# Optimization experiments

Hardware: AMD Instinct MI355X
Metric: run time of the kernel (lower is better)

Reference implementation:

```python
import jax, jax.numpy as jnp
import numpy as np

B, NB, S, K, M, C = 2, 6000, 3, 8, 6, 256
INIT = 0.02


def setup_inputs() -> dict:
    key = jax.random.key(0)
    ks = jax.random.split(key, 24)
    d = {}
    d["pts_query_feats"] = jax.random.normal(ks[0], (B, NB, C), jnp.float32)
    d["pts_query_pe"] = jax.random.normal(ks[1], (B, NB, C), jnp.float32)
    d["knn_feat_seq"] = jax.random.normal(ks[2], (S, B, NB, K, C), jnp.float32)
    d["knn_pe_seq"] = jax.random.normal(ks[3], (S, B, NB, K, C), jnp.float32)
    d["sampled_feat"] = jax.random.normal(ks[4], (B, NB, M, C), jnp.float32)
    d["mask"] = jax.random.bernoulli(ks[5], 0.7, (B, NB, M))  # True = valid image sample
    # per-seq temporal attention params (S cloned single-head MHA modules)
    d["Wq_t"] = INIT * jax.random.normal(ks[6], (S, C, C), jnp.float32)
    d["Wk_t"] = INIT * jax.random.normal(ks[7], (S, C, C), jnp.float32)
    d["Wv_t"] = INIT * jax.random.normal(ks[8], (S, C, C), jnp.float32)
    d["Wo_t"] = INIT * jax.random.normal(ks[9], (S, C, C), jnp.float32)
    d["bq_t"] = jnp.zeros((S, C), jnp.float32)
    d["bk_t"] = jnp.zeros((S, C), jnp.float32)
    d["bv_t"] = jnp.zeros((S, C), jnp.float32)
    d["bo_t"] = jnp.zeros((S, C), jnp.float32)
    # cross-sensor single-head MHA params
    d["Wq_c"] = INIT * jax.random.normal(ks[10], (C, C), jnp.float32)
    d["Wk_c"] = INIT * jax.random.normal(ks[11], (C, C), jnp.float32)
    d["Wv_c"] = INIT * jax.random.normal(ks[12], (C, C), jnp.float32)
    d["Wo_c"] = INIT * jax.random.normal(ks[13], (C, C), jnp.float32)
    d["bq_c"] = jnp.zeros((C,), jnp.float32)
    d["bk_c"] = jnp.zeros((C,), jnp.float32)
    d["bv_c"] = jnp.zeros((C,), jnp.float32)
    d["bo_c"] = jnp.zeros((C,), jnp.float32)
    return d


def reference(pts_query_feats, pts_query_pe, knn_feat_seq, knn_pe_seq,
              sampled_feat, mask,
              Wq_t, Wk_t, Wv_t, Wo_t, bq_t, bk_t, bv_t, bo_t,
              Wq_c, Wk_c, Wv_c, Wo_c, bq_c, bk_c, bv_c, bo_c):
    scale = 1.0 / np.sqrt(C).astype(np.float32)

    # with_pos_embed
    q_base = pts_query_feats + pts_query_pe           # [B,NB,C]
    kv = knn_feat_seq + knn_pe_seq                    # [S,B,NB,K,C]

    # temporal attention: per voxel, 1 query token attends over K knn keys;
    # S distinct (cloned) single-head MHA modules, outputs summed over seq.
    q = jnp.einsum('bnc,scd->sbnd', q_base, Wq_t) + bq_t[:, None, None, :]
    k = jnp.einsum('sbnkc,scd->sbnkd', kv, Wk_t) + bk_t[:, None, None, None, :]
    v = jnp.einsum('sbnkc,scd->sbnkd', kv, Wv_t) + bv_t[:, None, None, None, :]
    scores = jnp.einsum('sbnd,sbnkd->sbnk', q, k) * scale
    attn = jax.nn.softmax(scores, axis=-1)
    ctx = jnp.einsum('sbnk,sbnkd->sbnd', attn, v)
    out_s = jnp.einsum('sbnd,sde->sbne', ctx, Wo_t) + bo_t[:, None, None, :]
    out = out_s.sum(axis=0)                           # [B,NB,C]

    # cross-sensor attention over M image samples; attn_mask = ~mask (True blocks)
    valid = mask.any(axis=-1)                         # [B,NB]
    qc = out @ Wq_c + bq_c                            # [B,NB,C]
    kc = sampled_feat @ Wk_c + bk_c                   # [B,NB,M,C]
    vc = sampled_feat @ Wv_c + bv_c
    sc = jnp.einsum('bnc,bnmc->bnm', qc, kc) * scale
    sc = jnp.where(mask, sc, -1e9)
    a = jax.nn.softmax(sc, axis=-1)
    cctx = jnp.einsum('bnm,bnmc->bnc', a, vc)
    outc = cctx @ Wo_c + bo_c                         # [B,NB,C]

    # original drops invalid voxels; we keep static shape and zero them
    return jnp.where(valid[..., None], outc, 0.0)
```

## Files before the change

kernel.cpp:

```cpp
#include <hip/hip_runtime.h>
#include <math.h>

#define CC 256
#define KK 8
#define MM 6
#define SS 3
#define NVOX 12000
#define VB 16
#define NBLK (NVOX / VB)

typedef __attribute__((ext_vector_type(8))) short bf16x8;
typedef __attribute__((ext_vector_type(4))) float f32x4;
typedef __attribute__((ext_vector_type(4))) float fvec4;

#define OFF_QK3PK  0u
#define OFF_WBIGPK 393216u
#define OFF_WVOCPK 786432u
#define OFF_BQK    917504u
#define OFF_BBIG   920576u
#define OFF_BVOC   921600u
#define WS_NEED    922624u

__device__ __forceinline__ float wred(float p) {
  #pragma unroll
  for (int off = 32; off; off >>= 1) p += __shfl_xor(p, off, 64);
  return p;
}
__device__ __forceinline__ uint f2bf(float x) {
  const uint u = __float_as_uint(x);
  return (u + 0x7fffu + ((u >> 16) & 1u)) >> 16;
}
__device__ __forceinline__ uint bfpack(float a, float b) {
  return (f2bf(b) << 16) | f2bf(a);
}
__device__ __forceinline__ float bflo(uint w) { return __uint_as_float(w << 16); }
__device__ __forceinline__ float bfhi(uint w) { return __uint_as_float(w & 0xffff0000u); }

__device__ __forceinline__ f32x4 mfma16(bf16x8 a, bf16x8 b, f32x4 c) {
  return __builtin_amdgcn_mfma_f32_16x16x32_bf16(a, b, c, 0, 0, 0);
}

__global__ __launch_bounds__(256) void prep_all(
    const float* __restrict__ Wq_t, const float* __restrict__ Wq_c,
    const float* __restrict__ Wk_t, const float* __restrict__ Wk_c,
    const float* __restrict__ Wv_t, const float* __restrict__ Wv_c,
    const float* __restrict__ Wo_t, const float* __restrict__ Wo_c,
    const float* __restrict__ bq_t, const float* __restrict__ bq_c,
    const float* __restrict__ bv_t, const float* __restrict__ bv_c,
    const float* __restrict__ bo_t, const float* __restrict__ bo_c,
    uint4* __restrict__ qk3pk, uint4* __restrict__ wbigpk,
    uint4* __restrict__ wvocpk,
    float* __restrict__ bqk, float* __restrict__ bbig,
    float* __restrict__ bvoc) {
  const int b = blockIdx.x, t = threadIdx.x;
  __shared__ float xl[8][256];
  if (b < 96) {
    const int u = b >> 5, c0 = (b & 31) * 8;
    const float* Wq = Wq_t + u * 65536;
    const float* Wk = Wk_t + u * 65536;
    #pragma unroll
    for (int i = 0; i < 8; ++i) xl[i][t] = Wq[(c0 + i) * 256 + t];
    __syncthreads();
    float acc[8] = {0.f, 0.f, 0.f, 0.f, 0.f, 0.f, 0.f, 0.f};
    const float4* wr = (const float4*)(Wk + t * 256);
    #pragma unroll 4
    for (int d4 = 0; d4 < 64; ++d4) {
      const float4 wv = wr[d4];
      #pragma unroll
      for (int j = 0; j < 8; ++j)
        acc[j] += xl[j][d4 * 4] * wv.x + xl[j][d4 * 4 + 1] * wv.y +
                  xl[j][d4 * 4 + 2] * wv.z + xl[j][d4 * 4 + 3] * wv.w;
    }
    const int lane = (((c0 >> 3) & 3) << 4) | (t & 15);
    uint4 o;
    o.x = bfpack(acc[0], acc[1]); o.y = bfpack(acc[2], acc[3]);
    o.z = bfpack(acc[4], acc[5]); o.w = bfpack(acc[6], acc[7]);
    qk3pk[((u * 16 + (t >> 4)) * 8 + (c0 >> 5)) * 64 + lane] = o;
  } else if (b < 192) {
    const int v = (b - 96) >> 5, bi = (b - 96) & 31;
    const int c0 = bi * 8, row0 = v * 256 + c0;
    const float* Wv = Wv_t + v * 65536;
    const float* Wo = Wo_t + v * 65536;
    #pragma unroll
    for (int i = 0; i < 8; ++i) xl[i][t] = Wv[(c0 + i) * 256 + t];
    __syncthreads();
    float a1[8] = {0.f, 0.f, 0.f, 0.f, 0.f, 0.f, 0.f, 0.f};
    #pragma unroll 4
    for (int d = 0; d < 256; ++d) {
      const float w = Wo[d * 256 + t];
      #pragma unroll
      for (int j = 0; j < 8; ++j) a1[j] += xl[j][d] * w;
    }
    __syncthreads();
    #pragma unroll
    for (int j = 0; j < 8; ++j) xl[j][t] = a1[j];
    __syncthreads();
    float a2[8] = {0.f, 0.f, 0.f, 0.f, 0.f, 0.f, 0.f, 0.f};
    #pragma unroll 4
    for (int d = 0; d < 256; ++d) {
      const float w = Wq_c[d * 256 + t];
      #pragma unroll
      for (int j = 0; j < 8; ++j) a2[j] += xl[j][d] * w;
    }
    __syncthreads();
    #pragma unroll
    for (int j = 0; j < 8; ++j) xl[j][t] = a2[j];
    __syncthreads();
    float a3[8] = {0.f, 0.f, 0.f, 0.f, 0.f, 0.f, 0.f, 0.f};
    const float4* wr = (const float4*)(Wk_c + t * 256);
    #pragma unroll 4
    for (int d4 = 0; d4 < 64; ++d4) {
      const float4 wv = wr[d4];
      #pragma unroll
      for (int j = 0; j < 8; ++j)
        a3[j] += xl[j][d4 * 4] * wv.x + xl[j][d4 * 4 + 1] * wv.y +
                 xl[j][d4 * 4 + 2] * wv.z + xl[j][d4 * 4 + 3] * wv.w;
    }
    const int lane = (((row0 >> 3) & 3) << 4) | (t & 15);
    uint4 o;
    o.x = bfpack(a3[0], a3[1]); o.y = bfpack(a3[2], a3[3]);
    o.z = bfpack(a3[4], a3[5]); o.w = bfpack(a3[6], a3[7]);
    wbigpk[((t >> 4) * 24 + (row0 >> 5)) * 64 + lane] = o;
  } else if (b < 224) {
    const int c0 = (b - 192) * 8;
    #pragma unroll
    for (int i = 0; i < 8; ++i) xl[i][t] = Wv_c[(c0 + i) * 256 + t];
    __syncthreads();
    float acc[8] = {0.f, 0.f, 0.f, 0.f, 0.f, 0.f, 0.f, 0.f};
    #pragma unroll 4
    for (int d = 0; d < 256; ++d) {
      const float w = Wo_c[d * 256 + t];
      #pragma unroll
      for (int j = 0; j < 8; ++j) acc[j] += xl[j][d] * w;
    }
    const int lane = (((c0 >> 3) & 3) << 4) | (t & 15);
    uint4 o;
    o.x = bfpack(acc[0], acc[1]); o.y = bfpack(acc[2], acc[3]);
    o.z = bfpack(acc[4], acc[5]); o.w = bfpack(acc[6], acc[7]);
    wvocpk[((t >> 4) * 8 + (c0 >> 5)) * 64 + lane] = o;
  } else if (b < 227) {
    const int u = b - 224;
    xl[0][t] = bq_t[u * 256 + t];
    __syncthreads();
    const float4* wr = (const float4*)(Wk_t + u * 65536 + t * 256);
    float a = 0.f;
    #pragma unroll 4
    for (int d4 = 0; d4 < 64; ++d4) {
      const float4 wv = wr[d4];
      a += xl[0][d4 * 4] * wv.x + xl[0][d4 * 4 + 1] * wv.y +
           xl[0][d4 * 4 + 2] * wv.z + xl[0][d4 * 4 + 3] * wv.w;
    }
    bqk[u * 256 + t] = a;
  } else {
    xl[0][t] = bv_t[t]; xl[1][t] = bv_t[256 + t];
    xl[2][t] = bv_t[512 + t]; xl[3][t] = bv_c[t];
    __syncthreads();
    float bvs = bo_t[t] + bo_t[256 + t] + bo_t[512 + t];
    float bvc = bo_c[t];
    #pragma unroll 2
    for (int d = 0; d < 256; ++d) {
      bvs += xl[0][d] * Wo_t[d * 256 + t] +
             xl[1][d] * Wo_t[65536 + d * 256 + t] +
             xl[2][d] * Wo_t[131072 + d * 256 + t];
      bvc += xl[3][d] * Wo_c[d * 256 + t];
    }
    bvoc[t] = bvc;
    __syncthreads();
    xl[4][t] = bvs;
    __syncthreads();
    float y = bq_c[t];
    #pragma unroll 4
    for (int d = 0; d < 256; ++d) y += xl[4][d] * Wq_c[d * 256 + t];
    __syncthreads();
    xl[5][t] = y;
    __syncthreads();
    const float4* wr = (const float4*)(Wk_c + t * 256);
    float bb = 0.f;
    #pragma unroll 4
    for (int d4 = 0; d4 < 64; ++d4) {
      const float4 wv = wr[d4];
      bb += xl[5][d4 * 4] * wv.x + xl[5][d4 * 4 + 1] * wv.y +
            xl[5][d4 * 4 + 2] * wv.z + xl[5][d4 * 4 + 3] * wv.w;
    }
    bbig[t] = bb;
  }
}

__global__ __launch_bounds__(512, 6) void stftr_mega(
    const float* __restrict__ ptsf, const float* __restrict__ ptspe,
    const float* __restrict__ knnf, const float* __restrict__ knnpe,
    const float* __restrict__ sfeat, const int* __restrict__ maskp,
    const bf16x8* __restrict__ qk3pk, const bf16x8* __restrict__ wbigpk,
    const bf16x8* __restrict__ wvocpk,
    const float* __restrict__ bqk, const float* __restrict__ bbig,
    const float* __restrict__ bvoc,
    float* __restrict__ out) {
  __shared__ char shA[25088];
  __shared__ char shB[24832];
  __shared__ int mlds[VB * MM];
  __shared__ int vlds[VB];
  const int t = threadIdx.x, lane = t & 63, w = t >> 6;
  const int g0 = blockIdx.x * VB;

  {
    uint* qb_u = (uint*)shB;
    const fvec4* a4 = (const fvec4*)(ptsf + (size_t)g0 * CC);
    const fvec4* b4 = (const fvec4*)(ptspe + (size_t)g0 * CC);
    #pragma unroll
    for (int it = 0; it < 2; ++it) {
      const int idx = it * 512 + t;
      const int row = idx >> 6, c4 = idx & 63;
      const fvec4 va = __builtin_nontemporal_load(&a4[idx]);
      const fvec4 vb = __builtin_nontemporal_load(&b4[idx]);
      qb_u[row * 132 + c4 * 2]     = bfpack(va.x + vb.x, va.y + vb.y);
      qb_u[row * 132 + c4 * 2 + 1] = bfpack(va.z + vb.z, va.w + vb.w);
    }
    if (t < VB * MM) mlds[t] = maskp[g0 * MM + t];
  }
  __syncthreads();
  {
    f32x4 acc[6];
    #pragma unroll
    for (int nb = 0; nb < 6; ++nb) acc[nb] = (f32x4){0.f, 0.f, 0.f, 0.f};
    const char* qbase = shB + (lane & 15) * 528 + (lane >> 4) * 16;
    #pragma unroll
    for (int kb = 0; kb < 8; ++kb) {
      const bf16x8 a = *(const bf16x8*)(qbase + kb * 64);
      #pragma unroll
      for (int nb = 0; nb < 6; ++nb) {
        const bf16x8 bb = qk3pk[((w * 6 + nb) * 8 + kb) * 64 + lane];
        acc[nb] = mfma16(a, bb, acc[nb]);
      }
    }
    ushort* us = (ushort*)shA;
    #pragma unroll
    for (int nb = 0; nb < 6; ++nb) {
      const int n = (w * 6 + nb) * 16 + (lane & 15);
      const float bias = bqk[n];
      #pragma unroll
      for (int r = 0; r < 4; ++r) {
        const int row = (lane >> 4) * 4 + r;
        us[row * 776 + n] = (ushort)f2bf(acc[nb][r] + bias);
      }
    }
  }
  __syncthreads();
  {
    const uint* Au = (const uint*)shA;
    uint* Bu = (uint*)shB;
    const fvec4* kfp = (const fvec4*)knnf;
    const fvec4* kpp = (const fvec4*)knnpe;
    for (int q = 0; q < 6; ++q) {
      const int tid = w * 6 + q;
      const int s = tid >> 4, j = tid & 15;
      const size_t rb = ((size_t)(s * NVOX + g0 + j)) * 512 + lane;
      fvec4 sm[KK];
      #pragma unroll
      for (int r = 0; r < KK; ++r) {
        const fvec4 kf = __builtin_nontemporal_load(&kfp[rb + r * 64]);
        const fvec4 kp = __builtin_nontemporal_load(&kpp[rb + r * 64]);
        sm[r] = kf + kp;
      }
      const uint ua = Au[j * 388 + s * 128 + lane * 2];
      const uint ub = Au[j * 388 + s * 128 + lane * 2 + 1];
      const float u0 = bflo(ua), u1 = bfhi(ua), u2 = bflo(ub), u3 = bfhi(ub);
      float sc[KK];
      #pragma unroll
      for (int r = 0; r < KK; ++r) {
        float p = sm[r].x * u0 + sm[r].y * u1 + sm[r].z * u2 + sm[r].w * u3;
        sc[r] = wred(p);
      }
      float mx = sc[0];
      #pragma unroll
      for (int r = 1; r < KK; ++r) mx = fmaxf(mx, sc[r]);
      float e[KK], sum = 0.f;
      #pragma unroll
      for (int r = 0; r < KK; ++r) { e[r] = __expf((sc[r] - mx) * 0.0625f); sum += e[r]; }
      const float inv = 1.f / sum;
      fvec4 acc = (fvec4){0.f, 0.f, 0.f, 0.f};
      #pragma unroll
      for (int r = 0; r < KK; ++r) acc += (e[r] * inv) * sm[r];
      Bu[j * 388 + s * 128 + lane * 2]     = bfpack(acc.x, acc.y);
      Bu[j * 388 + s * 128 + lane * 2 + 1] = bfpack(acc.z, acc.w);
    }
  }
  __syncthreads();
  {
    f32x4 acc[2];
    acc[0] = (f32x4){0.f, 0.f, 0.f, 0.f};
    acc[1] = (f32x4){0.f, 0.f, 0.f, 0.f};
    const char* abase = shB + (lane & 15) * 1552 + (lane >> 4) * 16;
    #pragma unroll 4
    for (int kb = 0; kb < 24; ++kb) {
      const bf16x8 a = *(const bf16x8*)(abase + kb * 64);
      #pragma unroll
      for (int nb = 0; nb < 2; ++nb) {
        const bf16x8 bb = wbigpk[((w * 2 + nb) * 24 + kb) * 64 + lane];
        acc[nb] = mfma16(a, bb, acc[nb]);
      }
    }
    ushort* ust = (ushort*)shA;
    #pragma unroll
    for (int nb = 0; nb < 2; ++nb) {
      const int n = (w * 2 + nb) * 16 + (lane & 15);
      const float bias = bbig[n];
      #pragma unroll
      for (int r = 0; r < 4; ++r) {
        const int row = (lane >> 4) * 4 + r;
        ust[row * 264 + n] = (ushort)f2bf(acc[nb][r] + bias);
      }
    }
  }
  __syncthreads();
  {
    const uint* Au = (const uint*)shA;
    uint* Bu = (uint*)shB;
    const fvec4* sfp = (const fvec4*)sfeat;
    #pragma unroll
    for (int jj = 0; jj < 2; ++jj) {
      const int j = w * 2 + jj;
      const int g = g0 + j;
      const uint ua = Au[j * 132 + lane * 2];
      const uint ub = Au[j * 132 + lane * 2 + 1];
      const float u0 = bflo(ua), u1 = bfhi(ua), u2 = bflo(ub), u3 = bfhi(ub);
      const size_t sb = (size_t)g * (MM * 64) + lane;
      fvec4 sf[MM]; float scm[MM]; int anyv = 0;
      #pragma unroll
      for (int m = 0; m < MM; ++m) {
        sf[m] = __builtin_nontemporal_load(&sfp[sb + m * 64]);
        const int mk = mlds[j * MM + m];
        anyv |= mk;
        float p = sf[m].x * u0 + sf[m].y * u1 + sf[m].z * u2 + sf[m].w * u3;
        p = wred(p);
        scm[m] = mk ? p * 0.0625f : -1e9f;
      }
      float mx = scm[0];
      #pragma unroll
      for (int m = 1; m < MM; ++m) mx = fmaxf(mx, scm[m]);
      float e[MM], sum = 0.f;
      #pragma unroll
      for (int m = 0; m < MM; ++m) { e[m] = __expf(scm[m] - mx); sum += e[m]; }
      const float inv = 1.f / sum;
      fvec4 ag = (fvec4){0.f, 0.f, 0.f, 0.f};
      #pragma unroll
      for (int m = 0; m < MM; ++m) ag += (e[m] * inv) * sf[m];
      Bu[j * 132 + lane * 2]     = bfpack(ag.x, ag.y);
      Bu[j * 132 + lane * 2 + 1] = bfpack(ag.z, ag.w);
      if (lane == 0) vlds[j] = anyv;
    }
  }
  __syncthreads();
  {
    f32x4 acc[2];
    acc[0] = (f32x4){0.f, 0.f, 0.f, 0.f};
    acc[1] = (f32x4){0.f, 0.f, 0.f, 0.f};
    const char* cbase = shB + (lane & 15) * 528 + (lane >> 4) * 16;
    #pragma unroll
    for (int kb = 0; kb < 8; ++kb) {
      const bf16x8 a = *(const bf16x8*)(cbase + kb * 64);
      #pragma unroll
      for (int nb = 0; nb < 2; ++nb) {
        const bf16x8 bb = wvocpk[((w * 2 + nb) * 8 + kb) * 64 + lane];
        acc[nb] = mfma16(a, bb, acc[nb]);
      }
    }
    float* ost = (float*)(shA + 8448);
    #pragma unroll
    for (int nb = 0; nb < 2; ++nb) {
      const int n = (w * 2 + nb) * 16 + (lane & 15);
      const float bias = bvoc[n];
      #pragma unroll
      for (int r = 0; r < 4; ++r) {
        const int row = (lane >> 4) * 4 + r;
        ost[row * 260 + n] = acc[nb][r] + bias;
      }
    }
  }
  __syncthreads();
  {
    const float* ost = (const float*)(shA + 8448);
    #pragma unroll
    for (int it = 0; it < 8; ++it) {
      const int idx = it * 512 + t;
      const int row = idx >> 8, d = idx & 255;
      const float v = vlds[row] ? ost[row * 260 + d] : 0.f;
      __builtin_nontemporal_store(v, &out[((size_t)(g0 + row)) * 256 + d]);
    }
  }
}

extern "C" void kernel_launch(void* const* d_in, const int* in_sizes, int n_in,
                              void* d_out, int out_size, void* d_ws, size_t ws_size,
                              hipStream_t stream) {
  const float* ptsf  = (const float*)d_in[0];
  const float* ptspe = (const float*)d_in[1];
  const float* knnf  = (const float*)d_in[2];
  const float* knnpe = (const float*)d_in[3];
  const float* sfeat = (const float*)d_in[4];
  const int*   maskp = (const int*)d_in[5];
  const float* Wq_t = (const float*)d_in[6];
  const float* Wk_t = (const float*)d_in[7];
  const float* Wv_t = (const float*)d_in[8];
  const float* Wo_t = (const float*)d_in[9];
  const float* bq_t = (const float*)d_in[10];
  const float* bv_t = (const float*)d_in[12];
  const float* bo_t = (const float*)d_in[13];
  const float* Wq_c = (const float*)d_in[14];
  const float* Wk_c = (const float*)d_in[15];
  const float* Wv_c = (const float*)d_in[16];
  const float* Wo_c = (const float*)d_in[17];
  const float* bq_c = (const float*)d_in[18];
  const float* bv_c = (const float*)d_in[20];
  const float* bo_c = (const float*)d_in[21];

  if (ws_size < WS_NEED) return;
  char* ws = (char*)d_ws;
  uint4* qk3pk  = (uint4*)(ws + OFF_QK3PK);
  uint4* wbigpk = (uint4*)(ws + OFF_WBIGPK);
  uint4* wvocpk = (uint4*)(ws + OFF_WVOCPK);
  float* bqk    = (float*)(ws + OFF_BQK);
  float* bbig   = (float*)(ws + OFF_BBIG);
  float* bvoc   = (float*)(ws + OFF_BVOC);

  prep_all<<<228, 256, 0, stream>>>(
      Wq_t, Wq_c, Wk_t, Wk_c, Wv_t, Wv_c, Wo_t, Wo_c,
      bq_t, bq_c, bv_t, bv_c, bo_t, bo_c,
      qk3pk, wbigpk, wvocpk, bqk, bbig, bvoc);

  stftr_mega<<<NBLK, 512, 0, stream>>>(
      ptsf, ptspe, knnf, knnpe, sfeat, maskp,
      (const bf16x8*)qk3pk, (const bf16x8*)wbigpk, (const bf16x8*)wvocpk,
      bqk, bbig, bvoc, (float*)d_out);
}
```

Before: 170.2 us.

## Process temporal sequences one at a time to shrink shared memory footprint

Restructures the temporal attention stage into a loop over the S sequences: each iteration computes that sequence's folded query projection, runs the KNN softmax for it, and accumulates its contribution to the combined output projection in registers. Shared memory drops from about 50KB to about 33.5KB per block, and per-wave accumulator registers fall from six MFMA tiles to two, which should allow more resident blocks per CU. The cost is more barriers per block and smaller per-stage work, leaving less independent memory traffic in flight within a block.

Result: slower. 181.5 us (+6.7%).

```diff
diff --git a/kernel.cpp b/kernel.cpp
--- a/kernel.cpp
+++ b/kernel.cpp
@@ -20,6 +20,11 @@
 #define OFF_BBIG   920576u
 #define OFF_BVOC   921600u
 #define WS_NEED    922624u
+
+#define QB_OFF   0u
+#define US_OFF   8448u
+#define WG_OFF   16896u
+#define SH_SIZE  33536u
 
 __device__ __forceinline__ float wred(float p) {
   #pragma unroll
@@ -195,15 +200,15 @@
     const float* __restrict__ bqk, const float* __restrict__ bbig,
     const float* __restrict__ bvoc,
     float* __restrict__ out) {
-  __shared__ char shA[25088];
-  __shared__ char shB[24832];
+  __shared__ char sh[SH_SIZE];
   __shared__ int mlds[VB * MM];
   __shared__ int vlds[VB];
   const int t = threadIdx.x, lane = t & 63, w = t >> 6;
   const int g0 = blockIdx.x * VB;
+  const int l15 = lane & 15, lhi = lane >> 4;
 
   {
-    uint* qb_u = (uint*)shB;
+    uint* qb_u = (uint*)(sh + QB_OFF);
     const fvec4* a4 = (const fvec4*)(ptsf + (size_t)g0 * CC);
     const fvec4* b4 = (const fvec4*)(ptspe + (size_t)g0 * CC);
     #pragma unroll
@@ -218,103 +223,98 @@
     if (t < VB * MM) mlds[t] = maskp[g0 * MM + t];
   }
   __syncthreads();
+
+  f32x4 uc0 = (f32x4){0.f, 0.f, 0.f, 0.f};
+  f32x4 uc1 = (f32x4){0.f, 0.f, 0.f, 0.f};
+
+  #pragma unroll 1
+  for (int s = 0; s < SS; ++s) {
+    {
+      f32x4 a0 = (f32x4){0.f, 0.f, 0.f, 0.f};
+      f32x4 a1 = (f32x4){0.f, 0.f, 0.f, 0.f};
+      const char* qbase = sh + QB_OFF + l15 * 528 + lhi * 16;
+      #pragma unroll
+      for (int kb = 0; kb < 8; ++kb) {
+        const bf16x8 a = *(const bf16x8*)(qbase + kb * 64);
+        a0 = mfma16(a, qk3pk[((s * 16 + w * 2 + 0) * 8 + kb) * 64 + lane], a0);
+        a1 = mfma16(a, qk3pk[((s * 16 + w * 2 + 1) * 8 + kb) * 64 + lane], a1);
+      }
+      ushort* us = (ushort*)(sh + US_OFF);
+      const int n0 = (w * 2) * 16 + l15, n1 = n0 + 16;
+      const float b0 = bqk[s * 256 + n0], b1 = bqk[s * 256 + n1];
+      #pragma unroll
+      for (int r = 0; r < 4; ++r) {
+        const int row = lhi * 4 + r;
+        us[row * 264 + n0] = (ushort)f2bf(a0[r] + b0);
+        us[row * 264 + n1] = (ushort)f2bf(a1[r] + b1);
+      }
+    }
+    __syncthreads();
+    {
+      const uint* Au = (const uint*)(sh + US_OFF);
+      uint* Bu = (uint*)(sh + WG_OFF);
+      const fvec4* kfp = (const fvec4*)knnf;
+      const fvec4* kpp = (const fvec4*)knnpe;
+      for (int q = 0; q < 2; ++q) {
+        const int j = w * 2 + q;
+        const size_t rb = ((size_t)(s * NVOX + g0 + j)) * 512 + lane;
+        fvec4 sm[KK];
+        #pragma unroll
+        for (int r = 0; r < KK; ++r) {
+          const fvec4 kf = __builtin_nontemporal_load(&kfp[rb + r * 64]);
+          const fvec4 kp = __builtin_nontemporal_load(&kpp[rb + r * 64]);
+          sm[r] = kf + kp;
+        }
+        const uint ua = Au[j * 132 + lane * 2];
+        const uint ub = Au[j * 132 + lane * 2 + 1];
+        const float u0 = bflo(ua), u1 = bfhi(ua), u2 = bflo(ub), u3 = bfhi(ub);
+        float sc[KK];
+        #pragma unroll
+        for (int r = 0; r < KK; ++r) {
+          float p = sm[r].x * u0 + sm[r].y * u1 + sm[r].z * u2 + sm[r].w * u3;
+          sc[r] = wred(p);
+        }
+        float mx = sc[0];
+        #pragma unroll
+        for (int r = 1; r < KK; ++r) mx = fmaxf(mx, sc[r]);
+        float e[KK], sum = 0.f;
+        #pragma unroll
+        for (int r = 0; r < KK; ++r) { e[r] = __expf((sc[r] - mx) * 0.0625f); sum += e[r]; }
+        const float inv = 1.f / sum;
+        fvec4 acc = (fvec4){0.f, 0.f, 0.f, 0.f};
+        #pragma unroll
+        for (int r = 0; r < KK; ++r) acc += (e[r] * inv) * sm[r];
+        Bu[j * 132 + lane * 2]     = bfpack(acc.x, acc.y);
+        Bu[j * 132 + lane * 2 + 1] = bfpack(acc.z, acc.w);
+      }
+    }
+    __syncthreads();
+    {
+      const char* wbase = sh + WG_OFF + l15 * 528 + lhi * 16;
+      #pragma unroll
+      for (int kb = 0; kb < 8; ++kb) {
+        const bf16x8 a = *(const bf16x8*)(wbase + kb * 64);
+        uc0 = mfma16(a, wbigpk[((w * 2 + 0) * 24 + s * 8 + kb) * 64 + lane], uc0);
+        uc1 = mfma16(a, wbigpk[((w * 2 + 1) * 24 + s * 8 + kb) * 64 + lane], uc1);
+      }
+    }
+  }
+
   {
-    f32x4 acc[6];
-    #pragma unroll
-    for (int nb = 0; nb < 6; ++nb) acc[nb] = (f32x4){0.f, 0.f, 0.f, 0.f};
-    const char* qbase = shB + (lane & 15) * 528 + (lane >> 4) * 16;
-    #pragma unroll
-    for (int kb = 0; kb < 8; ++kb) {
-      const bf16x8 a = *(const bf16x8*)(qbase + kb * 64);
-      #pragma unroll
-      for (int nb = 0; nb < 6; ++nb) {
-        const bf16x8 bb = qk3pk[((w * 6 + nb) * 8 + kb) * 64 + lane];
-        acc[nb] = mfma16(a, bb, acc[nb]);
-      }
-    }
-    ushort* us = (ushort*)shA;
-    #pragma unroll
-    for (int nb = 0; nb < 6; ++nb) {
-      const int n = (w * 6 + nb) * 16 + (lane & 15);
-      const float bias = bqk[n];
-      #pragma unroll
-      for (int r = 0; r < 4; ++r) {
-        const int row = (lane >> 4) * 4 + r;
-        us[row * 776 + n] = (ushort)f2bf(acc[nb][r] + bias);
-      }
+    ushort* ust = (ushort*)(sh + QB_OFF);
+    const int n0 = (w * 2) * 16 + l15, n1 = n0 + 16;
+    const float b0 = bbig[n0], b1 = bbig[n1];
+    #pragma unroll
+    for (int r = 0; r < 4; ++r) {
+      const int row = lhi * 4 + r;
+      ust[row * 264 + n0] = (ushort)f2bf(uc0[r] + b0);
+      ust[row * 264 + n1] = (ushort)f2bf(uc1[r] + b1);
     }
   }
   __syncthreads();
   {
-    const uint* Au = (const uint*)shA;
-    uint* Bu = (uint*)shB;
-    const fvec4* kfp = (const fvec4*)knnf;
-    const fvec4* kpp = (const fvec4*)knnpe;
-    for (int q = 0; q < 6; ++q) {
-      const int tid = w * 6 + q;
-      const int s = tid >> 4, j = tid & 15;
-      const size_t rb = ((size_t)(s * NVOX + g0 + j)) * 512 + lane;
-      fvec4 sm[KK];
-      #pragma unroll
-      for (int r = 0; r < KK; ++r) {
-        const fvec4 kf = __builtin_nontemporal_load(&kfp[rb + r * 64]);
-        const fvec4 kp = __builtin_nontemporal_load(&kpp[rb + r * 64]);
-        sm[r] = kf + kp;
-      }
-      const uint ua = Au[j * 388 + s * 128 + lane * 2];
-      const uint ub = Au[j * 388 + s * 128 + lane * 2 + 1];
-      const float u0 = bflo(ua), u1 = bfhi(ua), u2 = bflo(ub), u3 = bfhi(ub);
-      float sc[KK];
-      #pragma unroll
-      for (int r = 0; r < KK; ++r) {
-        float p = sm[r].x * u0 + sm[r].y * u1 + sm[r].z * u2 + sm[r].w * u3;
-        sc[r] = wred(p);
-      }
-      float mx = sc[0];
-      #pragma unroll
-      for (int r = 1; r < KK; ++r) mx = fmaxf(mx, sc[r]);
-      float e[KK], sum = 0.f;
-      #pragma unroll
-      for (int r = 0; r < KK; ++r) { e[r] = __expf((sc[r] - mx) * 0.0625f); sum += e[r]; }
-      const float inv = 1.f / sum;
-      fvec4 acc = (fvec4){0.f, 0.f, 0.f, 0.f};
-      #pragma unroll
-      for (int r = 0; r < KK; ++r) acc += (e[r] * inv) * sm[r];
-      Bu[j * 388 + s * 128 + lane * 2]     = bfpack(acc.x, acc.y);
-      Bu[j * 388 + s * 128 + lane * 2 + 1] = bfpack(acc.z, acc.w);
-    }
-  }
-  __syncthreads();
-  {
-    f32x4 acc[2];
-    acc[0] = (f32x4){0.f, 0.f, 0.f, 0.f};
-    acc[1] = (f32x4){0.f, 0.f, 0.f, 0.f};
-    const char* abase = shB + (lane & 15) * 1552 + (lane >> 4) * 16;
-    #pragma unroll 4
-    for (int kb = 0; kb < 24; ++kb) {
-      const bf16x8 a = *(const bf16x8*)(abase + kb * 64);
-      #pragma unroll
-      for (int nb = 0; nb < 2; ++nb) {
-        const bf16x8 bb = wbigpk[((w * 2 + nb) * 24 + kb) * 64 + lane];
-        acc[nb] = mfma16(a, bb, acc[nb]);
-      }
-    }
-    ushort* ust = (ushort*)shA;
-    #pragma unroll
-    for (int nb = 0; nb < 2; ++nb) {
-      const int n = (w * 2 + nb) * 16 + (lane & 15);
-      const float bias = bbig[n];
-      #pragma unroll
-      for (int r = 0; r < 4; ++r) {
-        const int row = (lane >> 4) * 4 + r;
-        ust[row * 264 + n] = (ushort)f2bf(acc[nb][r] + bias);
-      }
-    }
-  }
-  __syncthreads();
-  {
-    const uint* Au = (const uint*)shA;
-    uint* Bu = (uint*)shB;
+    const uint* Au = (const uint*)(sh + QB_OFF);
+    uint* Bu = (uint*)(sh + US_OFF);
     const fvec4* sfp = (const fvec4*)sfeat;
     #pragma unroll
     for (int jj = 0; jj < 2; ++jj) {
@@ -351,34 +351,28 @@
   }
   __syncthreads();
   {
-    f32x4 acc[2];
-    acc[0] = (f32x4){0.f, 0.f, 0.f, 0.f};
-    acc[1] = (f32x4){0.f, 0.f, 0.f, 0.f};
-    const char* cbase = shB + (lane & 15) * 528 + (lane >> 4) * 16;
+    f32x4 a0 = (f32x4){0.f, 0.f, 0.f, 0.f};
+    f32x4 a1 = (f32x4){0.f, 0.f, 0.f, 0.f};
+    const char* cbase = sh + US_OFF + l15 * 528 + lhi * 16;
     #pragma unroll
     for (int kb = 0; kb < 8; ++kb) {
       const bf16x8 a = *(const bf16x8*)(cbase + kb * 64);
-      #pragma unroll
-      for (int nb = 0; nb < 2; ++nb) {
-        const bf16x8 bb = wvocpk[((w * 2 + nb) * 8 + kb) * 64 + lane];
-        acc[nb] = mfma16(a, bb, acc[nb]);
-      }
-    }
-    float* ost = (float*)(shA + 8448);
-    #pragma unroll
-    for (int nb = 0; nb < 2; ++nb) {
-      const int n = (w * 2 + nb) * 16 + (lane & 15);
-      const float bias = bvoc[n];
-      #pragma unroll
-      for (int r = 0; r < 4; ++r) {
-        const int row = (lane >> 4) * 4 + r;
-        ost[row * 260 + n] = acc[nb][r] + bias;
-      }
+      a0 = mfma16(a, wvocpk[((w * 2 + 0) * 8 + kb) * 64 + lane], a0);
+      a1 = mfma16(a, wvocpk[((w * 2 + 1) * 8 + kb) * 64 + lane], a1);
+    }
+    float* ost = (float*)(sh + WG_OFF);
+    const int n0 = (w * 2) * 16 + l15, n1 = n0 + 16;
+    const float b0 = bvoc[n0], b1 = bvoc[n1];
+    #pragma unroll
+    for (int r = 0; r < 4; ++r) {
+      const int row = lhi * 4 + r;
+      ost[row * 260 + n0] = a0[r] + b0;
+      ost[row * 260 + n1] = a1[r] + b1;
     }
   }
   __syncthreads();
   {
-    const float* ost = (const float*)(shA + 8448);
+    const float* ost = (const float*)(sh + WG_OFF);
     #pragma unroll
     for (int it = 0; it < 8; ++it) {
       const int idx = it * 512 + t;
```

## Software-pipeline KNN and sampled-feature loads into registers across stages

Applied to the files above, without the earlier changes.

Issues the first voxel's KNN feature and PE loads before the query projection, then prefetches the next voxel's KNN rows while the current one is processed. On the last iteration it prefetches the sampled image features for the cross-sensor stage. This hides global memory latency behind compute. It raises register pressure a lot (about 64 extra vec4 registers), so the launch bound's minimum occupancy is lowered from 6 to 4 blocks' worth of waves.

Result: slower. 184.7 us (+8.5%).

```diff
diff --git a/kernel.cpp b/kernel.cpp
--- a/kernel.cpp
+++ b/kernel.cpp
@@ -186,7 +186,7 @@
   }
 }
 
-__global__ __launch_bounds__(512, 6) void stftr_mega(
+__global__ __launch_bounds__(512, 4) void stftr_mega(
     const float* __restrict__ ptsf, const float* __restrict__ ptspe,
     const float* __restrict__ knnf, const float* __restrict__ knnpe,
     const float* __restrict__ sfeat, const int* __restrict__ maskp,
@@ -201,6 +201,21 @@
   __shared__ int vlds[VB];
   const int t = threadIdx.x, lane = t & 63, w = t >> 6;
   const int g0 = blockIdx.x * VB;
+  const fvec4* kfp = (const fvec4*)knnf;
+  const fvec4* kpp = (const fvec4*)knnpe;
+  const fvec4* sfp = (const fvec4*)sfeat;
+
+  fvec4 pkf[KK], pkp[KK];
+  {
+    const int tid0 = w * 6;
+    const int s0 = tid0 >> 4, j0 = tid0 & 15;
+    const size_t rb0 = ((size_t)(s0 * NVOX + g0 + j0)) * 512 + lane;
+    #pragma unroll
+    for (int r = 0; r < KK; ++r) {
+      pkf[r] = __builtin_nontemporal_load(&kfp[rb0 + r * 64]);
+      pkp[r] = __builtin_nontemporal_load(&kpp[rb0 + r * 64]);
+    }
+  }
 
   {
     uint* qb_u = (uint*)shB;
@@ -245,21 +260,35 @@
     }
   }
   __syncthreads();
+  fvec4 psf[2][MM];
   {
     const uint* Au = (const uint*)shA;
     uint* Bu = (uint*)shB;
-    const fvec4* kfp = (const fvec4*)knnf;
-    const fvec4* kpp = (const fvec4*)knnpe;
+    #pragma unroll
     for (int q = 0; q < 6; ++q) {
       const int tid = w * 6 + q;
       const int s = tid >> 4, j = tid & 15;
-      const size_t rb = ((size_t)(s * NVOX + g0 + j)) * 512 + lane;
       fvec4 sm[KK];
       #pragma unroll
-      for (int r = 0; r < KK; ++r) {
-        const fvec4 kf = __builtin_nontemporal_load(&kfp[rb + r * 64]);
-        const fvec4 kp = __builtin_nontemporal_load(&kpp[rb + r * 64]);
-        sm[r] = kf + kp;
+      for (int r = 0; r < KK; ++r) sm[r] = pkf[r] + pkp[r];
+      if (q < 5) {
+        const int tid1 = tid + 1;
+        const int s1 = tid1 >> 4, j1 = tid1 & 15;
+        const size_t rb1 = ((size_t)(s1 * NVOX + g0 + j1)) * 512 + lane;
+        #pragma unroll
+        for (int r = 0; r < KK; ++r) {
+          pkf[r] = __builtin_nontemporal_load(&kfp[rb1 + r * 64]);
+          pkp[r] = __builtin_nontemporal_load(&kpp[rb1 + r * 64]);
+        }
+      } else {
+        #pragma unroll
+        for (int jj = 0; jj < 2; ++jj) {
+          const int g = g0 + w * 2 + jj;
+          const size_t sb = (size_t)g * (MM * 64) + lane;
+          #pragma unroll
+          for (int m = 0; m < MM; ++m)
+            psf[jj][m] = __builtin_nontemporal_load(&sfp[sb + m * 64]);
+        }
       }
       const uint ua = Au[j * 388 + s * 128 + lane * 2];
       const uint ub = Au[j * 388 + s * 128 + lane * 2 + 1];
@@ -315,22 +344,19 @@
   {
     const uint* Au = (const uint*)shA;
     uint* Bu = (uint*)shB;
-    const fvec4* sfp = (const fvec4*)sfeat;
     #pragma unroll
     for (int jj = 0; jj < 2; ++jj) {
       const int j = w * 2 + jj;
-      const int g = g0 + j;
       const uint ua = Au[j * 132 + lane * 2];
       const uint ub = Au[j * 132 + lane * 2 + 1];
       const float u0 = bflo(ua), u1 = bfhi(ua), u2 = bflo(ub), u3 = bfhi(ub);
-      const size_t sb = (size_t)g * (MM * 64) + lane;
-      fvec4 sf[MM]; float scm[MM]; int anyv = 0;
+      float scm[MM]; int anyv = 0;
       #pragma unroll
       for (int m = 0; m < MM; ++m) {
-        sf[m] = __builtin_nontemporal_load(&sfp[sb + m * 64]);
+        const fvec4 sf = psf[jj][m];
         const int mk = mlds[j * MM + m];
         anyv |= mk;
-        float p = sf[m].x * u0 + sf[m].y * u1 + sf[m].z * u2 + sf[m].w * u3;
+        float p = sf.x * u0 + sf.y * u1 + sf.z * u2 + sf.w * u3;
         p = wred(p);
         scm[m] = mk ? p * 0.0625f : -1e9f;
       }
@@ -343,7 +369,7 @@
       const float inv = 1.f / sum;
       fvec4 ag = (fvec4){0.f, 0.f, 0.f, 0.f};
       #pragma unroll
-      for (int m = 0; m < MM; ++m) ag += (e[m] * inv) * sf[m];
+      for (int m = 0; m < MM; ++m) ag += (e[m] * inv) * psf[jj][m];
       Bu[j * 132 + lane * 2]     = bfpack(ag.x, ag.y);
       Bu[j * 132 + lane * 2 + 1] = bfpack(ag.z, ag.w);
       if (lane == 0) vlds[j] = anyv;
```
